# Kernel tuning notes

Measured on AMD Instinct MI355X. Metric: run time of the kernel, lower is better.

Reference implementation:

```python
import jax, jax.numpy as jnp
import numpy as np

B, L, D, H = 4, 2048, 1024, 16
DK = D // H  # 64


def setup_inputs() -> dict:
    key = jax.random.key(0)
    ks = jax.random.split(key, 5)
    scale = 1.0 / np.sqrt(D)
    return {
        "x": jax.random.normal(ks[0], (B, L, D), dtype=jnp.float32),
        "Wq": jax.random.normal(ks[1], (D, D), dtype=jnp.float32) * scale,
        "Wk": jax.random.normal(ks[2], (D, D), dtype=jnp.float32) * scale,
        "Wv": jax.random.normal(ks[3], (D, D), dtype=jnp.float32) * scale,
        "Wo": jax.random.normal(ks[4], (D, D), dtype=jnp.float32) * scale,
    }


def reference(x, Wq, Wk, Wv, Wo):
    b, l, d = x.shape
    # Linear: y = x @ W^T (weight stored as [out, in], no bias)
    def proj(W):
        y = jnp.einsum('bld,ed->ble', x, W)            # [B,L,D]
        return y.reshape(b, l, H, DK).transpose(0, 2, 1, 3)  # [B,H,L,dk]
    Q, K, V = proj(Wq), proj(Wk), proj(Wv)
    scores = jnp.einsum('bhqd,bhkd->bhqk', Q, K) / jnp.sqrt(jnp.float32(DK))
    causal = jnp.tril(jnp.ones((l, l), dtype=bool))
    scores = jnp.where(causal[None, None, :, :], scores, jnp.float32(-1e30))
    attn = jax.nn.softmax(scores, axis=-1)             # stable softmax
    out = jnp.einsum('bhqk,bhkd->bhqd', attn, V)       # [B,H,L,dk]
    out = out.transpose(0, 2, 1, 3).reshape(b, l, d)   # [B,L,D]
    return jnp.einsum('bld,ed->ble', out, Wo)
```

## Files before the change

### kernel.cpp

```cpp
#include <hip/hip_runtime.h>
#include <hip/hip_bf16.h>
#include <stdint.h>

typedef short bf16x8 __attribute__((ext_vector_type(8)));
typedef float f32x4 __attribute__((ext_vector_type(4)));
typedef float f32x16 __attribute__((ext_vector_type(16)));
typedef unsigned int uint4v __attribute__((ext_vector_type(4)));

#define NB 4
#define NL 2048
#define ND 1024
#define NH 16
#define NDK 64
#define NM (NB*NL)
#define QSCALE 0.18033688011112042f

__device__ __forceinline__ ushort f2bf(float f) {
  __bf16 h = (__bf16)f;
  return __builtin_bit_cast(unsigned short, h);
}

__device__ __forceinline__ unsigned int cvtpk(float lo, float hi) {
  unsigned int d;
  asm("v_cvt_pk_bf16_f32 %0, %1, %2" : "=v"(d) : "v"(lo), "v"(hi));
  return d;
}

__device__ __forceinline__ void gload16(const void* g, void* l) {
  __builtin_amdgcn_global_load_lds(
      (__attribute__((address_space(1))) void*)(uintptr_t)g,
      (__attribute__((address_space(3))) void*)(uint32_t)(uintptr_t)l,
      16, 0, 0);
}

__device__ __forceinline__ f32x16 mfma32(bf16x8 a, bf16x8 b, f32x16 c) {
  return __builtin_amdgcn_mfma_f32_32x32x16_bf16(a, b, c, 0, 0, 0);
}
__device__ __forceinline__ f32x4 mfma16(bf16x8 a, bf16x8 b, f32x4 c) {
  return __builtin_amdgcn_mfma_f32_16x16x32_bf16(a, b, c, 0, 0, 0);
}

__global__ void convert_all(const float* __restrict__ x, const float* __restrict__ wq,
                            const float* __restrict__ wk, const float* __restrict__ wv,
                            const float* __restrict__ wo, ushort* __restrict__ o) {
  long i = (long)blockIdx.x * 256 + threadIdx.x;
  const long NX = 2097152;
  const long NW = 262144;
  const float4* s;
  long off;
  if (i < NX) { s = (const float4*)x; off = i; }
  else {
    long j = i - NX;
    int wsel = (int)(j >> 18);
    off = j & (NW - 1);
    s = (const float4*)(wsel == 0 ? wq : wsel == 1 ? wk : wsel == 2 ? wv : wo);
  }
  float4 v = s[off];
  ushort4 r;
  r.x = f2bf(v.x); r.y = f2bf(v.y); r.z = f2bf(v.z); r.w = f2bf(v.w);
  ((ushort4*)o)[i] = r;
}

template<int MODE>
__global__ __launch_bounds__(256, 2)
void gemm_bt(const ushort* __restrict__ A,
             const ushort* __restrict__ Bq, const ushort* __restrict__ Bk, const ushort* __restrict__ Bv,
             ushort* __restrict__ Oq, ushort* __restrict__ Ok, ushort* __restrict__ Ov,
             float* __restrict__ OF) {
  __shared__ __align__(16) ushort lA[2][128 * 32];
  __shared__ __align__(16) ushort lB[2][128 * 32];
  const int t = threadIdx.x;
  const int w = t >> 6, l = t & 63;
  const int lr = l & 15, lh = l >> 4;
  const int bxr = blockIdx.x;
  const int bx = (bxr & 7) * 8 + (bxr >> 3);
  const int m0 = bx * 128;
  const int ng = blockIdx.y * 128;
  const ushort* Bp;
  ushort* Op = nullptr;
  int mi = 0, n0;
  if (MODE == 0) {
    mi = ng >> 10;
    Bp = (mi == 0) ? Bq : (mi == 1) ? Bk : Bv;
    Op = (mi == 0) ? Oq : (mi == 1) ? Ok : Ov;
    n0 = ng & 1023;
  } else {
    Bp = Bq;
    n0 = ng;
  }
  const int wrow = (w >> 1) * 64, wcol = (w & 1) * 64;
  const int r = t >> 2, c = t & 3;
  const ushort* gA0 = A + (size_t)(m0 + r) * ND + c * 8;
  const ushort* gA1 = A + (size_t)(m0 + 64 + r) * ND + c * 8;
  const ushort* gB0 = Bp + (size_t)(n0 + r) * ND + c * 8;
  const ushort* gB1 = Bp + (size_t)(n0 + 64 + r) * ND + c * 8;

#define GSTAGE(bi, kofs) do {                              \
    gload16(gA0 + (kofs), &lA[bi][w * 512]);               \
    gload16(gA1 + (kofs), &lA[bi][2048 + w * 512]);        \
    gload16(gB0 + (kofs), &lB[bi][w * 512]);               \
    gload16(gB1 + (kofs), &lB[bi][2048 + w * 512]);        \
  } while (0)

  GSTAGE(0, 0);
  f32x4 acc[4][4] = {};
  for (int kt = 0; kt < ND; kt += 32) {
    const int buf = (kt >> 5) & 1;
    __syncthreads();
    if (kt + 32 < ND) GSTAGE(buf ^ 1, kt + 32);
    bf16x8 af[4], bfr[4];
#pragma unroll
    for (int mt = 0; mt < 4; mt++)
      af[mt] = *(const bf16x8*)&lA[buf][(wrow + mt * 16 + lr) * 32 + lh * 8];
#pragma unroll
    for (int nt = 0; nt < 4; nt++)
      bfr[nt] = *(const bf16x8*)&lB[buf][(wcol + nt * 16 + lr) * 32 + lh * 8];
#pragma unroll
    for (int mt = 0; mt < 4; mt++)
#pragma unroll
      for (int nt = 0; nt < 4; nt++)
        acc[mt][nt] = mfma16(af[mt], bfr[nt], acc[mt][nt]);
  }
#undef GSTAGE
#pragma unroll
  for (int mt = 0; mt < 4; mt++) {
#pragma unroll
    for (int nt = 0; nt < 4; nt++) {
#pragma unroll
      for (int j = 0; j < 4; j++) {
        int m = m0 + wrow + mt * 16 + lh * 4 + j;
        int n = wcol + nt * 16 + lr;
        if (MODE == 0) {
          int nl = n0 + n;
          int b = m >> 11, ll = m & 2047;
          int h = nl >> 6, dk = nl & 63;
          float v = acc[mt][nt][j];
          if (mi == 0) v *= QSCALE;
          if (mi == 2)
            Op[(((size_t)(b * NH + h)) * NDK + dk) * NL + ll] = f2bf(v);
          else
            Op[(((size_t)(b * NH + h)) * NL + ll) * NDK + dk] = f2bf(v);
        } else {
          OF[(size_t)m * ND + ng + n] = acc[mt][nt][j];
        }
      }
    }
  }
}

__global__ __launch_bounds__(256, 4)
void attn_fwd(const ushort* __restrict__ Q, const ushort* __restrict__ Kg,
              const ushort* __restrict__ VT, ushort* __restrict__ O) {
  __shared__ __align__(16) ushort lK[2][64 * 64];
  __shared__ __align__(16) ushort lV[2][64 * 64];
  const int t = threadIdx.x;
  const int w = t >> 6, l = t & 63;
  const int l31 = l & 31, hi = l >> 5;
  const int id = blockIdx.x;
  const int bh = id & 63;
  const int g = (id >> 6) & 3;
  const int k4 = id >> 8;
  const int qt = (k4 == 0) ? g : (k4 == 1) ? 7 - g : (k4 == 2) ? 8 + g : 15 - g;
  const size_t base = (size_t)bh * (NL * NDK);
  const int q0w = qt * 128 + w * 32;
  const int ktmax = q0w >> 6;
  const int NT = qt * 2 + 2;

  bf16x8 qf[4];
  {
    const ushort* qp = Q + base + (size_t)(q0w + l31) * NDK + hi * 8;
#pragma unroll
    for (int sl = 0; sl < 4; sl++) qf[sl] = *(const bf16x8*)(qp + sl * 16);
  }

  const int kr0 = t >> 3, kc0 = (t & 7) ^ (kr0 & 7);
  const int s1i = t + 256;
  const int kr1 = s1i >> 3, kc1 = (s1i & 7) ^ (kr1 & 7);
  const ushort* gK0 = Kg + base + (size_t)kr0 * NDK + kc0 * 8;
  const ushort* gK1 = Kg + base + (size_t)kr1 * NDK + kc1 * 8;
  const ushort* gV0 = VT + base + (size_t)kr0 * NL + kc0 * 8;
  const ushort* gV1 = VT + base + (size_t)kr1 * NL + kc1 * 8;

  float l_run = 0.f;
  f32x16 accO0 = {}, accO1 = {};
  const int swz = l31 & 7;

#define STAGE(bufi, kt1) do {                                       \
    const size_t kvn = (size_t)(kt1) * 64;                          \
    gload16(gK0 + kvn * NDK, &lK[bufi][w * 512]);                   \
    gload16(gK1 + kvn * NDK, &lK[bufi][2048 + w * 512]);            \
    gload16(gV0 + kvn, &lV[bufi][w * 512]);                         \
    gload16(gV1 + kvn, &lV[bufi][2048 + w * 512]);                  \
  } while (0)

  STAGE(0, 0);

  for (int kt = 0; kt < NT; kt++) {
    const int buf = kt & 1;
    __syncthreads();
    if (kt + 1 < NT) STAGE(buf ^ 1, kt + 1);
    if (kt <= ktmax) {
      const int kv0 = kt * 64;
      const ushort* bK = lK[buf];
      const ushort* bV = lV[buf];
      f32x16 s0 = {}, s1v = {};
      __builtin_amdgcn_s_setprio(1);
#pragma unroll
      for (int sl = 0; sl < 4; sl++) {
        int c = 2 * sl + hi;
        bf16x8 kf0 = *(const bf16x8*)&bK[l31 * 64 + ((c ^ swz) * 8)];
        bf16x8 kf1 = *(const bf16x8*)&bK[(32 + l31) * 64 + ((c ^ swz) * 8)];
        s0 = mfma32(kf0, qf[sl], s0);
        s1v = mfma32(kf1, qf[sl], s1v);
      }
      __builtin_amdgcn_s_setprio(0);
      if (kt == ktmax) {
        const int qrel = q0w + l31 - kv0;
#pragma unroll
        for (int r = 0; r < 16; r++) {
          int kvo = (r & 3) + 8 * (r >> 2) + 4 * hi;
          if (kvo > qrel) s0[r] = -1e30f;
          if (kvo + 32 > qrel) s1v[r] = -1e30f;
        }
      }
      float sum = 0.f;
#pragma unroll
      for (int r = 0; r < 16; r++) { s0[r] = exp2f(s0[r]); sum += s0[r]; }
#pragma unroll
      for (int r = 0; r < 16; r++) { s1v[r] = exp2f(s1v[r]); sum += s1v[r]; }
      l_run += sum;
      bf16x8 pa[4];
#pragma unroll
      for (int ks = 0; ks < 4; ks++) {
        const int k2 = (ks & 1) * 8;
        unsigned int a0, a1, b0, b1;
        if (ks >> 1) {
          a0 = cvtpk(s1v[k2 + 0], s1v[k2 + 1]); a1 = cvtpk(s1v[k2 + 2], s1v[k2 + 3]);
          b0 = cvtpk(s1v[k2 + 4], s1v[k2 + 5]); b1 = cvtpk(s1v[k2 + 6], s1v[k2 + 7]);
        } else {
          a0 = cvtpk(s0[k2 + 0], s0[k2 + 1]); a1 = cvtpk(s0[k2 + 2], s0[k2 + 3]);
          b0 = cvtpk(s0[k2 + 4], s0[k2 + 5]); b1 = cvtpk(s0[k2 + 6], s0[k2 + 7]);
        }
        unsigned int a0s = __shfl_xor(a0, 32), a1s = __shfl_xor(a1, 32);
        unsigned int b0s = __shfl_xor(b0, 32), b1s = __shfl_xor(b1, 32);
        uint4v pd;
        pd[0] = hi ? b0s : a0;
        pd[1] = hi ? b1s : a1;
        pd[2] = hi ? b0 : a0s;
        pd[3] = hi ? b1 : a1s;
        pa[ks] = __builtin_bit_cast(bf16x8, pd);
      }
      __builtin_amdgcn_s_setprio(1);
#pragma unroll
      for (int ks = 0; ks < 4; ks++) {
        int c = 2 * ks + hi;
        bf16x8 vf0 = *(const bf16x8*)&bV[l31 * 64 + ((c ^ swz) * 8)];
        bf16x8 vf1 = *(const bf16x8*)&bV[(32 + l31) * 64 + ((c ^ swz) * 8)];
        accO0 = mfma32(vf0, pa[ks], accO0);
        accO1 = mfma32(vf1, pa[ks], accO1);
      }
      __builtin_amdgcn_s_setprio(0);
    }
  }
#undef STAGE
  l_run += __shfl_xor(l_run, 32);
  const int b = bh >> 4, h = bh & 15;
  const float inv = 1.0f / l_run;
  const int q = q0w + l31;
  ushort* orow = O + ((size_t)b * NL + q) * ND + h * NDK;
#pragma unroll
  for (int gi = 0; gi < 4; gi++) {
    ushort4 o0, o1;
    o0.x = f2bf(accO0[4 * gi + 0] * inv); o0.y = f2bf(accO0[4 * gi + 1] * inv);
    o0.z = f2bf(accO0[4 * gi + 2] * inv); o0.w = f2bf(accO0[4 * gi + 3] * inv);
    o1.x = f2bf(accO1[4 * gi + 0] * inv); o1.y = f2bf(accO1[4 * gi + 1] * inv);
    o1.z = f2bf(accO1[4 * gi + 2] * inv); o1.w = f2bf(accO1[4 * gi + 3] * inv);
    *(ushort4*)&orow[8 * gi + 4 * hi] = o0;
    *(ushort4*)&orow[32 + 8 * gi + 4 * hi] = o1;
  }
}

extern "C" void kernel_launch(void* const* d_in, const int* in_sizes, int n_in,
                              void* d_out, int out_size, void* d_ws, size_t ws_size,
                              hipStream_t stream) {
  const float* x = (const float*)d_in[0];
  const float* wq = (const float*)d_in[1];
  const float* wk = (const float*)d_in[2];
  const float* wv = (const float*)d_in[3];
  const float* wo = (const float*)d_in[4];
  char* ws = (char*)d_ws;
  ushort* xb  = (ushort*)(ws);
  ushort* wqb = (ushort*)(ws + 16777216);
  ushort* wkb = (ushort*)(ws + 18874368);
  ushort* wvb = (ushort*)(ws + 20971520);
  ushort* wob = (ushort*)(ws + 23068672);
  ushort* Qb  = (ushort*)(ws + 25165824);
  ushort* Kb  = (ushort*)(ws + 41943040);
  ushort* Vb  = (ushort*)(ws + 58720256);
  ushort* Ob  = (ushort*)(ws + 75497472);

  convert_all<<<12288, 256, 0, stream>>>(x, wq, wk, wv, wo, xb);
  gemm_bt<0><<<dim3(64, 24), 256, 0, stream>>>(xb, wqb, wkb, wvb, Qb, Kb, Vb, nullptr);
  attn_fwd<<<dim3(1024), 256, 0, stream>>>(Qb, Kb, Vb, Ob);
  gemm_bt<1><<<dim3(64, 8), 256, 0, stream>>>(Ob, wob, nullptr, nullptr,
                                              nullptr, nullptr, nullptr, (float*)d_out);
}
```

Baseline: 177.1 us.

## Split KV loop across two wave groups per block with LDS reduction

```diff
diff --git a/kernel.cpp b/kernel.cpp
--- a/kernel.cpp
+++ b/kernel.cpp
@@ -148,23 +148,24 @@
   }
 }
 
-__global__ __launch_bounds__(256, 4)
+__global__ __launch_bounds__(512, 4)
 void attn_fwd(const ushort* __restrict__ Q, const ushort* __restrict__ Kg,
               const ushort* __restrict__ VT, ushort* __restrict__ O) {
-  __shared__ __align__(16) ushort lK[2][64 * 64];
-  __shared__ __align__(16) ushort lV[2][64 * 64];
+  __shared__ __align__(16) ushort lKV[8][64 * 64];
   const int t = threadIdx.x;
   const int w = t >> 6, l = t & 63;
   const int l31 = l & 31, hi = l >> 5;
+  const int tau = w >> 2;
+  const int wi = w & 3;
   const int id = blockIdx.x;
   const int bh = id & 63;
-  const int g = (id >> 6) & 3;
-  const int k4 = id >> 8;
-  const int qt = (k4 == 0) ? g : (k4 == 1) ? 7 - g : (k4 == 2) ? 8 + g : 15 - g;
+  const int j = id >> 6;
+  const int qt = (j < 8) ? (15 - j) : (j - 8);
   const size_t base = (size_t)bh * (NL * NDK);
-  const int q0w = qt * 128 + w * 32;
+  const int q0w = qt * 128 + wi * 32;
   const int ktmax = q0w >> 6;
   const int NT = qt * 2 + 2;
+  const int P = qt + 1;
 
   bf16x8 qf[4];
   {
@@ -173,36 +174,28 @@
     for (int sl = 0; sl < 4; sl++) qf[sl] = *(const bf16x8*)(qp + sl * 16);
   }
 
-  const int kr0 = t >> 3, kc0 = (t & 7) ^ (kr0 & 7);
-  const int s1i = t + 256;
-  const int kr1 = s1i >> 3, kc1 = (s1i & 7) ^ (kr1 & 7);
-  const ushort* gK0 = Kg + base + (size_t)kr0 * NDK + kc0 * 8;
-  const ushort* gK1 = Kg + base + (size_t)kr1 * NDK + kc1 * 8;
-  const ushort* gV0 = VT + base + (size_t)kr0 * NL + kc0 * 8;
-  const ushort* gV1 = VT + base + (size_t)kr1 * NL + kc1 * 8;
+  const int kr = t >> 3, kc = (t & 7) ^ (kr & 7);
+  const ushort* gK = Kg + base + (size_t)kr * NDK + kc * 8;
+  const ushort* gV = VT + base + (size_t)kr * NL + kc * 8;
 
   float l_run = 0.f;
   f32x16 accO0 = {}, accO1 = {};
   const int swz = l31 & 7;
 
-#define STAGE(bufi, kt1) do {                                       \
-    const size_t kvn = (size_t)(kt1) * 64;                          \
-    gload16(gK0 + kvn * NDK, &lK[bufi][w * 512]);                   \
-    gload16(gK1 + kvn * NDK, &lK[bufi][2048 + w * 512]);            \
-    gload16(gV0 + kvn, &lV[bufi][w * 512]);                         \
-    gload16(gV1 + kvn, &lV[bufi][2048 + w * 512]);                  \
-  } while (0)
-
-  STAGE(0, 0);
-
-  for (int kt = 0; kt < NT; kt++) {
-    const int buf = kt & 1;
+#define STAGE1(tt) do { if ((tt) < NT) {                              \
+    gload16(gK + (size_t)(tt) * 64 * NDK, &lKV[(tt) & 3][w * 512]);   \
+    gload16(gV + (size_t)(tt) * 64,       &lKV[4 + ((tt) & 3)][w * 512]); } } while (0)
+
+  STAGE1(0); STAGE1(1);
+
+  for (int p = 0; p < P; p++) {
     __syncthreads();
-    if (kt + 1 < NT) STAGE(buf ^ 1, kt + 1);
-    if (kt <= ktmax) {
-      const int kv0 = kt * 64;
-      const ushort* bK = lK[buf];
-      const ushort* bV = lV[buf];
+    STAGE1(2 * p + 2);
+    STAGE1(2 * p + 3);
+    const int tt = 2 * p + tau;
+    if (tt <= ktmax) {
+      const ushort* bK = lKV[tt & 3];
+      const ushort* bV = lKV[4 + (tt & 3)];
       f32x16 s0 = {}, s1v = {};
       __builtin_amdgcn_s_setprio(1);
 #pragma unroll
@@ -214,8 +207,8 @@
         s1v = mfma32(kf1, qf[sl], s1v);
       }
       __builtin_amdgcn_s_setprio(0);
-      if (kt == ktmax) {
-        const int qrel = q0w + l31 - kv0;
+      if (tt == ktmax) {
+        const int qrel = q0w + l31 - tt * 64;
 #pragma unroll
         for (int r = 0; r < 16; r++) {
           int kvo = (r & 3) + 8 * (r >> 2) + 4 * hi;
@@ -262,21 +255,35 @@
       __builtin_amdgcn_s_setprio(0);
     }
   }
-#undef STAGE
-  l_run += __shfl_xor(l_run, 32);
-  const int b = bh >> 4, h = bh & 15;
-  const float inv = 1.0f / l_run;
-  const int q = q0w + l31;
-  ushort* orow = O + ((size_t)b * NL + q) * ND + h * NDK;
-#pragma unroll
-  for (int gi = 0; gi < 4; gi++) {
-    ushort4 o0, o1;
-    o0.x = f2bf(accO0[4 * gi + 0] * inv); o0.y = f2bf(accO0[4 * gi + 1] * inv);
-    o0.z = f2bf(accO0[4 * gi + 2] * inv); o0.w = f2bf(accO0[4 * gi + 3] * inv);
-    o1.x = f2bf(accO1[4 * gi + 0] * inv); o1.y = f2bf(accO1[4 * gi + 1] * inv);
-    o1.z = f2bf(accO1[4 * gi + 2] * inv); o1.w = f2bf(accO1[4 * gi + 3] * inv);
-    *(ushort4*)&orow[8 * gi + 4 * hi] = o0;
-    *(ushort4*)&orow[32 + 8 * gi + 4 * hi] = o1;
+#undef STAGE1
+  __syncthreads();
+  float* red = (float*)&lKV[0][0];
+  const int ridx = (wi * 64 + l) * 33;
+  if (tau == 1) {
+#pragma unroll
+    for (int r = 0; r < 16; r++) { red[ridx + r] = accO0[r]; red[ridx + 16 + r] = accO1[r]; }
+    red[ridx + 32] = l_run;
+  }
+  __syncthreads();
+  if (tau == 0) {
+#pragma unroll
+    for (int r = 0; r < 16; r++) { accO0[r] += red[ridx + r]; accO1[r] += red[ridx + 16 + r]; }
+    l_run += red[ridx + 32];
+    l_run += __shfl_xor(l_run, 32);
+    const int b = bh >> 4, h = bh & 15;
+    const float inv = 1.0f / l_run;
+    const int q = q0w + l31;
+    ushort* orow = O + ((size_t)b * NL + q) * ND + h * NDK;
+#pragma unroll
+    for (int gi = 0; gi < 4; gi++) {
+      ushort4 o0, o1;
+      o0.x = f2bf(accO0[4 * gi + 0] * inv); o0.y = f2bf(accO0[4 * gi + 1] * inv);
+      o0.z = f2bf(accO0[4 * gi + 2] * inv); o0.w = f2bf(accO0[4 * gi + 3] * inv);
+      o1.x = f2bf(accO1[4 * gi + 0] * inv); o1.y = f2bf(accO1[4 * gi + 1] * inv);
+      o1.z = f2bf(accO1[4 * gi + 2] * inv); o1.w = f2bf(accO1[4 * gi + 3] * inv);
+      *(ushort4*)&orow[8 * gi + 4 * hi] = o0;
+      *(ushort4*)&orow[32 + 8 * gi + 4 * hi] = o1;
+    }
   }
 }
 
@@ -301,7 +308,7 @@
 
   convert_all<<<12288, 256, 0, stream>>>(x, wq, wk, wv, wo, xb);
   gemm_bt<0><<<dim3(64, 24), 256, 0, stream>>>(xb, wqb, wkb, wvb, Qb, Kb, Vb, nullptr);
-  attn_fwd<<<dim3(1024), 256, 0, stream>>>(Qb, Kb, Vb, Ob);
+  attn_fwd<<<dim3(1024), 512, 0, stream>>>(Qb, Kb, Vb, Ob);
   gemm_bt<1><<<dim3(64, 8), 256, 0, stream>>>(Ob, wob, nullptr, nullptr,
                                               nullptr, nullptr, nullptr, (float*)d_out);
 }
```

Measured after the change: 178.9 us. Within noise of the previous version (+1.0%).
